# Kernel optimization log

Measured on AMD Instinct MI355X. Metric: run time of the kernel, lower is better.

## Reference

```python
import jax, jax.numpy as jnp
import numpy as np

B, S, H, F, E = 2, 2048, 1024, 4096, 8  # batch, seq, hidden, ffn, num_experts


def setup_inputs() -> dict:
    key = jax.random.key(0)
    ks = jax.random.split(key, 4)
    x = jax.random.normal(ks[0], (B, S, H), dtype=jnp.float32)
    w_router = jax.random.normal(ks[1], (H, E), dtype=jnp.float32) * 0.02
    w1 = jax.random.normal(ks[2], (E, H, F), dtype=jnp.float32) * 0.02
    b1 = jnp.zeros((E, F), dtype=jnp.float32)
    w2 = jax.random.normal(ks[3], (E, F, H), dtype=jnp.float32) * 0.02
    b2 = jnp.zeros((E, H), dtype=jnp.float32)
    return {"x": x, "w_router": w_router, "w1": w1, "b1": b1, "w2": w2, "b2": b2}


def reference(x, w_router, w1, b1, w2, b2):
    """Top-1 MoE layer: route -> per-expert FFN -> weighted combine.

    Faithful to ExpertParallelWrapper._process_moe_layer on a single group:
    router picks one expert per token with a routing weight; tokens are
    dispatched to experts (here expressed as a static mask over the fixed
    expert set), processed by the expert FFN, and scatter-combined back
    weighted by the routing probability.
    """
    Bs, Ss, Hs = x.shape
    n_experts = w1.shape[0]
    # Router: per-token logits -> softmax -> top-1 expert + weight
    logits = jnp.einsum('bsh,he->bse', x, w_router)          # [B,S,E]
    probs = jax.nn.softmax(logits, axis=-1)
    sel = jnp.argmax(probs, axis=-1)                          # [B,S] selected expert
    wgt = jnp.take_along_axis(probs, sel[..., None], axis=-1)[..., 0]  # [B,S]

    xt = x.reshape(-1, Hs)        # [T,H] flat tokens
    sel_t = sel.reshape(-1)       # [T]
    wgt_t = wgt.reshape(-1)       # [T]

    out = jnp.zeros_like(xt)
    # Static loop over the small fixed expert set (dispatch/combine via mask).
    for e in range(n_experts):
        h = jax.nn.relu(xt @ w1[e] + b1[e])   # [T,F]
        y = h @ w2[e] + b2[e]                 # [T,H]
        m = (sel_t == e).astype(xt.dtype) * wgt_t
        out = out + m[:, None] * y
    return out.reshape(Bs, Ss, Hs)
```

## Files before the change

kernel.cpp:

```cpp
#include <hip/hip_runtime.h>
#include <math.h>

#define T_TOK 4096
#define H_DIM 1024
#define F_DIM 4096
#define E_NUM 8
#define BK 64
#define KSPLIT 4

typedef __attribute__((ext_vector_type(8))) short bhalf8_t;
typedef __attribute__((ext_vector_type(8))) unsigned short ushort8_t;
typedef __attribute__((ext_vector_type(4))) float f32x4_t;

__device__ __forceinline__ unsigned short f2bf(float f) {
  unsigned int u = __float_as_uint(f);
  return (unsigned short)((u + 0x7fffu + ((u >> 16) & 1u)) >> 16);
}

__device__ __forceinline__ void gload16(const void* g, void* l) {
  __builtin_amdgcn_global_load_lds(
      (const __attribute__((address_space(1))) unsigned int*)g,
      (__attribute__((address_space(3))) unsigned int*)l, 16, 0, 0);
}

__device__ __forceinline__ void transpose_dev(const float* __restrict__ src,
                                              unsigned short* __restrict__ dst,
                                              int K, int N, int bx, int by, void* sm_) {
  float(*tile)[65] = (float(*)[65])sm_;
  const int n0 = bx * 64;
  const int k0 = by * 64;
  const int l = threadIdx.x;
  const int lr = l >> 4;
  const int lc = (l & 15) * 4;
#pragma unroll
  for (int i = 0; i < 64; i += 16) {
    const float4 v = *reinterpret_cast<const float4*>(&src[(size_t)(k0 + lr + i) * N + n0 + lc]);
    tile[lr + i][lc] = v.x;
    tile[lr + i][lc + 1] = v.y;
    tile[lr + i][lc + 2] = v.z;
    tile[lr + i][lc + 3] = v.w;
  }
  __syncthreads();
  const int kk = (l & 7) * 8;
  const int nr = l >> 3;
#pragma unroll
  for (int i = 0; i < 64; i += 32) {
    const int n = nr + i;
    ushort8_t o;
#pragma unroll
    for (int j = 0; j < 8; ++j) o[j] = f2bf(tile[kk + j][n]);
    *reinterpret_cast<ushort8_t*>(&dst[(size_t)(n0 + n) * K + k0 + kk]) = o;
  }
}

__global__ __launch_bounds__(256) void k_pre(const float* __restrict__ x,
                                             const float* __restrict__ wr,
                                             const float* __restrict__ w1,
                                             unsigned short* __restrict__ WT1,
                                             int* __restrict__ sel, float* __restrict__ wgt) {
  __shared__ __align__(16) char sm[64 * 65 * 4];
  if (blockIdx.x < 64) {
    transpose_dev(w1 + (size_t)blockIdx.z * H_DIM * F_DIM,
                  WT1 + (size_t)blockIdx.z * F_DIM * H_DIM,
                  H_DIM, F_DIM, blockIdx.x, blockIdx.y, sm);
    return;
  }
  if (blockIdx.z != 0) return;
  const int bid = blockIdx.y * 64 + (blockIdx.x - 64);
  const int t = bid * 4 + (threadIdx.x >> 6);
  const int lane = threadIdx.x & 63;
  const float* xr = x + (size_t)t * H_DIM;
  double acc[E_NUM] = {0, 0, 0, 0, 0, 0, 0, 0};
  for (int h = lane; h < H_DIM; h += 64) {
    const double xv = (double)xr[h];
    const float* w = wr + (size_t)h * E_NUM;
#pragma unroll
    for (int e = 0; e < E_NUM; ++e) acc[e] += xv * (double)w[e];
  }
#pragma unroll
  for (int e = 0; e < E_NUM; ++e) {
#pragma unroll
    for (int off = 32; off > 0; off >>= 1) acc[e] += __shfl_down(acc[e], off, 64);
  }
  if (lane == 0) {
    double m = acc[0];
    int a = 0;
#pragma unroll
    for (int e = 1; e < E_NUM; ++e)
      if (acc[e] > m) { m = acc[e]; a = e; }
    double s = 0.0;
#pragma unroll
    for (int e = 0; e < E_NUM; ++e) s += exp(acc[e] - m);
    sel[t] = a;
    wgt[t] = (float)(1.0 / s);
  }
}

__global__ void k_prefix(const int* __restrict__ sel, int* __restrict__ offs,
                         int* __restrict__ cursors) {
  __shared__ int h[E_NUM];
  if (threadIdx.x < E_NUM) h[threadIdx.x] = 0;
  __syncthreads();
  for (int i = threadIdx.x; i < T_TOK; i += 256) atomicAdd(&h[sel[i]], 1);
  __syncthreads();
  if (threadIdx.x == 0) {
    int s = 0;
    for (int e = 0; e < E_NUM; ++e) {
      offs[e] = s;
      cursors[e] = s;
      s += h[e];
    }
    offs[E_NUM] = s;
  }
}

__global__ void k_scatter(const float* __restrict__ x, const int* __restrict__ sel,
                          const float* __restrict__ wgt, int* __restrict__ cursors,
                          int* __restrict__ s2t, float* __restrict__ wgtS,
                          int* __restrict__ eS, unsigned short* __restrict__ Xs) {
  const int t = blockIdx.x;
  __shared__ int sslot;
  if (threadIdx.x == 0) {
    const int e = sel[t];
    const int slot = atomicAdd(&cursors[e], 1);
    sslot = slot;
    s2t[slot] = t;
    wgtS[slot] = wgt[t];
    eS[slot] = e;
  }
  __syncthreads();
  const int slot = sslot;
  const float4 v = reinterpret_cast<const float4*>(x + (size_t)t * H_DIM)[threadIdx.x];
  ushort4 o;
  o.x = f2bf(v.x); o.y = f2bf(v.y); o.z = f2bf(v.z); o.w = f2bf(v.w);
  reinterpret_cast<ushort4*>(Xs + (size_t)slot * H_DIM)[threadIdx.x] = o;
}

__global__ __launch_bounds__(256, 4) void k_mid(const unsigned short* __restrict__ Xs,
                                                const unsigned short* __restrict__ Wt,
                                                const float* __restrict__ b1,
                                                unsigned short* __restrict__ Hws,
                                                const int* __restrict__ offs,
                                                const float* __restrict__ w2,
                                                unsigned short* __restrict__ WT2) {
  __shared__ __align__(16) char sm[32768];
  if (blockIdx.x >= 32) {
    const int id = blockIdx.y * 32 + (blockIdx.x - 32);
    transpose_dev(w2 + (size_t)blockIdx.z * F_DIM * H_DIM,
                  WT2 + (size_t)blockIdx.z * H_DIM * F_DIM,
                  F_DIM, H_DIM, id & 15, id >> 4, sm);
    return;
  }
  const int e = blockIdx.z;
  const int off = offs[e];
  const int cnt = offs[e + 1] - off;
  const int m0 = blockIdx.y * 128;
  if (m0 >= cnt) return;
  const int n0 = blockIdx.x * 128;
  const int msize = cnt - m0;

  short* lA = (short*)sm;
  short* lB = (short*)(sm + 16384);

  const int tid = threadIdx.x;
  const int lane = tid & 63;
  const int wv = tid >> 6;
  const int wm = (wv >> 1) * 64;
  const int wn = (wv & 1) * 64;

  const int sRow = lane >> 3;
  const int cc = lane & 7;
  const int gch = cc ^ sRow;

  const unsigned short* Abase = Xs + (size_t)off * H_DIM;
  const unsigned short* Bbase = Wt + (size_t)e * F_DIM * H_DIM + (size_t)n0 * H_DIM;

  f32x4_t acc[4][4];
#pragma unroll
  for (int i = 0; i < 4; ++i)
#pragma unroll
    for (int j = 0; j < 4; ++j) acc[i][j] = (f32x4_t){0.f, 0.f, 0.f, 0.f};

  const int q = lane >> 4;
  const int r16 = lane & 15;
  const int sw = r16 & 7;

  for (int k0 = 0; k0 < H_DIM; k0 += BK) {
    __syncthreads();
#pragma unroll
    for (int i = 0; i < 4; ++i) {
      const int g = wv * 4 + i;
      const int row = g * 8 + sRow;
      const int ar = (row < msize) ? row : 0;
      gload16(Abase + (size_t)(m0 + ar) * H_DIM + k0 + gch * 8, &lA[g * 8 * BK]);
      gload16(Bbase + (size_t)row * H_DIM + k0 + gch * 8, &lB[g * 8 * BK]);
    }
    __syncthreads();

#pragma unroll
    for (int step = 0; step < 2; ++step) {
      const int slot = (step * 4 + q) ^ sw;
      bhalf8_t af[4], bf[4];
#pragma unroll
      for (int mi = 0; mi < 4; ++mi)
        af[mi] = *reinterpret_cast<const bhalf8_t*>(&lA[(wm + mi * 16 + r16) * BK + slot * 8]);
#pragma unroll
      for (int ni = 0; ni < 4; ++ni)
        bf[ni] = *reinterpret_cast<const bhalf8_t*>(&lB[(wn + ni * 16 + r16) * BK + slot * 8]);
#pragma unroll
      for (int mi = 0; mi < 4; ++mi)
#pragma unroll
        for (int ni = 0; ni < 4; ++ni)
          acc[mi][ni] = __builtin_amdgcn_mfma_f32_16x16x32_bf16(af[mi], bf[ni], acc[mi][ni], 0, 0, 0);
    }
  }

  const int c = lane & 15;
#pragma unroll
  for (int ni = 0; ni < 4; ++ni) {
    const int col = n0 + wn + ni * 16 + c;
    const float bias = b1[e * F_DIM + col];
#pragma unroll
    for (int mi = 0; mi < 4; ++mi) {
      const int rbase = wm + mi * 16 + q * 4;
#pragma unroll
      for (int r = 0; r < 4; ++r) {
        const int row = rbase + r;
        if (row < msize) {
          float v = acc[mi][ni][r] + bias;
          v = fmaxf(v, 0.0f);
          Hws[(size_t)(off + m0 + row) * F_DIM + col] = f2bf(v);
        }
      }
    }
  }
}

__global__ __launch_bounds__(256, 4) void k_ffn2_sk(const unsigned short* __restrict__ Hws,
                                                    const unsigned short* __restrict__ Wt,
                                                    const int* __restrict__ offs,
                                                    float* __restrict__ P) {
  const int e = blockIdx.z >> 2;
  const int ks = blockIdx.z & 3;
  const int off = offs[e];
  const int cnt = offs[e + 1] - off;
  const int m0 = blockIdx.y * 128;
  if (m0 >= cnt) return;
  const int n0 = blockIdx.x * 128;
  const int msize = cnt - m0;
  const int kbeg = ks * (F_DIM / KSPLIT);
  const int kend = kbeg + (F_DIM / KSPLIT);

  __shared__ short lA[128 * BK];
  __shared__ short lB[128 * BK];

  const int tid = threadIdx.x;
  const int lane = tid & 63;
  const int wv = tid >> 6;
  const int wm = (wv >> 1) * 64;
  const int wn = (wv & 1) * 64;

  const int sRow = lane >> 3;
  const int cc = lane & 7;
  const int gch = cc ^ sRow;

  const unsigned short* Abase = Hws + (size_t)off * F_DIM;
  const unsigned short* Bbase = Wt + (size_t)e * H_DIM * F_DIM + (size_t)n0 * F_DIM;

  f32x4_t acc[4][4];
#pragma unroll
  for (int i = 0; i < 4; ++i)
#pragma unroll
    for (int j = 0; j < 4; ++j) acc[i][j] = (f32x4_t){0.f, 0.f, 0.f, 0.f};

  const int q = lane >> 4;
  const int r16 = lane & 15;
  const int sw = r16 & 7;

  for (int k0 = kbeg; k0 < kend; k0 += BK) {
    __syncthreads();
#pragma unroll
    for (int i = 0; i < 4; ++i) {
      const int g = wv * 4 + i;
      const int row = g * 8 + sRow;
      const int ar = (row < msize) ? row : 0;
      gload16(Abase + (size_t)(m0 + ar) * F_DIM + k0 + gch * 8, &lA[g * 8 * BK]);
      gload16(Bbase + (size_t)row * F_DIM + k0 + gch * 8, &lB[g * 8 * BK]);
    }
    __syncthreads();

#pragma unroll
    for (int step = 0; step < 2; ++step) {
      const int slot = (step * 4 + q) ^ sw;
      bhalf8_t af[4], bf[4];
#pragma unroll
      for (int mi = 0; mi < 4; ++mi)
        af[mi] = *reinterpret_cast<const bhalf8_t*>(&lA[(wm + mi * 16 + r16) * BK + slot * 8]);
#pragma unroll
      for (int ni = 0; ni < 4; ++ni)
        bf[ni] = *reinterpret_cast<const bhalf8_t*>(&lB[(wn + ni * 16 + r16) * BK + slot * 8]);
#pragma unroll
      for (int mi = 0; mi < 4; ++mi)
#pragma unroll
        for (int ni = 0; ni < 4; ++ni)
          acc[mi][ni] = __builtin_amdgcn_mfma_f32_16x16x32_bf16(af[mi], bf[ni], acc[mi][ni], 0, 0, 0);
    }
  }

  const int c = lane & 15;
  float* Pb = P + (size_t)ks * T_TOK * H_DIM;
#pragma unroll
  for (int mi = 0; mi < 4; ++mi) {
    const int rbase = wm + mi * 16 + q * 4;
#pragma unroll
    for (int r = 0; r < 4; ++r) {
      const int row = rbase + r;
      if (row >= msize) continue;
      float* prow = Pb + (size_t)(off + m0 + row) * H_DIM;
#pragma unroll
      for (int ni = 0; ni < 4; ++ni) prow[n0 + wn + ni * 16 + c] = acc[mi][ni][r];
    }
  }
}

__global__ __launch_bounds__(256) void k_reduce(const float* __restrict__ P,
                                                const float* __restrict__ b2,
                                                const int* __restrict__ s2t,
                                                const int* __restrict__ eS,
                                                const float* __restrict__ wgtS,
                                                float* __restrict__ out) {
  const int srow = blockIdx.x;
  const int tok = s2t[srow];
  const int e = eS[srow];
  const float w = wgtS[srow];
  const int i = threadIdx.x;
  const size_t rowoff = (size_t)srow * H_DIM / 4 + i;
  const float4 p0 = reinterpret_cast<const float4*>(P)[rowoff];
  const float4 p1 = reinterpret_cast<const float4*>(P + (size_t)T_TOK * H_DIM)[rowoff];
  const float4 p2 = reinterpret_cast<const float4*>(P + (size_t)2 * T_TOK * H_DIM)[rowoff];
  const float4 p3 = reinterpret_cast<const float4*>(P + (size_t)3 * T_TOK * H_DIM)[rowoff];
  const float4 b = reinterpret_cast<const float4*>(b2 + (size_t)e * H_DIM)[i];
  float4 o;
  o.x = w * (p0.x + p1.x + p2.x + p3.x + b.x);
  o.y = w * (p0.y + p1.y + p2.y + p3.y + b.y);
  o.z = w * (p0.z + p1.z + p2.z + p3.z + b.z);
  o.w = w * (p0.w + p1.w + p2.w + p3.w + b.w);
  reinterpret_cast<float4*>(out + (size_t)tok * H_DIM)[i] = o;
}

__global__ __launch_bounds__(256) void k_transpose(const float* __restrict__ in,
                                                   unsigned short* __restrict__ out,
                                                   int K, int N) {
  __shared__ __align__(16) char sm[64 * 65 * 4];
  transpose_dev(in + (size_t)blockIdx.z * K * N, out + (size_t)blockIdx.z * N * K,
                K, N, blockIdx.x, blockIdx.y, sm);
}

__global__ __launch_bounds__(256, 4) void k_ffn2_direct(const unsigned short* __restrict__ Hws,
                                                        const unsigned short* __restrict__ Wt,
                                                        const float* __restrict__ b2,
                                                        const int* __restrict__ offs,
                                                        const int* __restrict__ s2t,
                                                        const float* __restrict__ wgtS,
                                                        float* __restrict__ out) {
  const int e = blockIdx.z;
  const int off = offs[e];
  const int cnt = offs[e + 1] - off;
  const int m0 = blockIdx.y * 128;
  if (m0 >= cnt) return;
  const int n0 = blockIdx.x * 128;
  const int msize = cnt - m0;

  __shared__ short lA[128 * BK];
  __shared__ short lB[128 * BK];

  const int tid = threadIdx.x;
  const int lane = tid & 63;
  const int wv = tid >> 6;
  const int wm = (wv >> 1) * 64;
  const int wn = (wv & 1) * 64;

  const int sRow = lane >> 3;
  const int cc = lane & 7;
  const int gch = cc ^ sRow;

  const unsigned short* Abase = Hws + (size_t)off * F_DIM;
  const unsigned short* Bbase = Wt + (size_t)e * H_DIM * F_DIM + (size_t)n0 * F_DIM;

  f32x4_t acc[4][4];
#pragma unroll
  for (int i = 0; i < 4; ++i)
#pragma unroll
    for (int j = 0; j < 4; ++j) acc[i][j] = (f32x4_t){0.f, 0.f, 0.f, 0.f};

  const int q = lane >> 4;
  const int r16 = lane & 15;
  const int sw = r16 & 7;

  for (int k0 = 0; k0 < F_DIM; k0 += BK) {
    __syncthreads();
#pragma unroll
    for (int i = 0; i < 4; ++i) {
      const int g = wv * 4 + i;
      const int row = g * 8 + sRow;
      const int ar = (row < msize) ? row : 0;
      gload16(Abase + (size_t)(m0 + ar) * F_DIM + k0 + gch * 8, &lA[g * 8 * BK]);
      gload16(Bbase + (size_t)row * F_DIM + k0 + gch * 8, &lB[g * 8 * BK]);
    }
    __syncthreads();

#pragma unroll
    for (int step = 0; step < 2; ++step) {
      const int slot = (step * 4 + q) ^ sw;
      bhalf8_t af[4], bf[4];
#pragma unroll
      for (int mi = 0; mi < 4; ++mi)
        af[mi] = *reinterpret_cast<const bhalf8_t*>(&lA[(wm + mi * 16 + r16) * BK + slot * 8]);
#pragma unroll
      for (int ni = 0; ni < 4; ++ni)
        bf[ni] = *reinterpret_cast<const bhalf8_t*>(&lB[(wn + ni * 16 + r16) * BK + slot * 8]);
#pragma unroll
      for (int mi = 0; mi < 4; ++mi)
#pragma unroll
        for (int ni = 0; ni < 4; ++ni)
          acc[mi][ni] = __builtin_amdgcn_mfma_f32_16x16x32_bf16(af[mi], bf[ni], acc[mi][ni], 0, 0, 0);
    }
  }

  const int c = lane & 15;
#pragma unroll
  for (int mi = 0; mi < 4; ++mi) {
    const int rbase = wm + mi * 16 + q * 4;
#pragma unroll
    for (int r = 0; r < 4; ++r) {
      const int row = rbase + r;
      if (row >= msize) continue;
      const int srow = off + m0 + row;
      const int tok = s2t[srow];
      const float w = wgtS[srow];
      float* orow = out + (size_t)tok * H_DIM;
#pragma unroll
      for (int ni = 0; ni < 4; ++ni) {
        const int col = n0 + wn + ni * 16 + c;
        orow[col] = w * (acc[mi][ni][r] + b2[e * H_DIM + col]);
      }
    }
  }
}

extern "C" void kernel_launch(void* const* d_in, const int* in_sizes, int n_in,
                              void* d_out, int out_size, void* d_ws, size_t ws_size,
                              hipStream_t stream) {
  const float* x  = (const float*)d_in[0];
  const float* wr = (const float*)d_in[1];
  const float* w1 = (const float*)d_in[2];
  const float* b1 = (const float*)d_in[3];
  const float* w2 = (const float*)d_in[4];
  const float* b2 = (const float*)d_in[5];
  float* out = (float*)d_out;

  char* ws = (char*)d_ws;
  const size_t NEED_FAST = 67108864ull * 2 + 8388608 + 33554432 + 98304;
  if (ws_size >= NEED_FAST) {
    unsigned short* WT1 = (unsigned short*)(ws);
    unsigned short* WT2 = (unsigned short*)(ws + 67108864);
    unsigned short* XS  = (unsigned short*)(ws + 134217728);
    unsigned short* HWS = (unsigned short*)(ws + 142606336);
    char* ctrl = ws + 176160768;
    int*   sel     = (int*)(ctrl);
    int*   s2t     = (int*)(ctrl + 16384);
    float* wgt     = (float*)(ctrl + 32768);
    float* wgtS    = (float*)(ctrl + 49152);
    int*   eS      = (int*)(ctrl + 65536);
    int*   offs    = (int*)(ctrl + 81920);
    int*   cursors = (int*)(ctrl + 81984);
    float* P = (float*)ws;

    k_pre<<<dim3(128, 16, 8), 256, 0, stream>>>(x, wr, w1, WT1, sel, wgt);
    k_prefix<<<1, 256, 0, stream>>>(sel, offs, cursors);
    k_scatter<<<T_TOK, 256, 0, stream>>>(x, sel, wgt, cursors, s2t, wgtS, eS, XS);
    k_mid<<<dim3(64, 32, 8), 256, 0, stream>>>(XS, WT1, b1, HWS, offs, w2, WT2);
    k_ffn2_sk<<<dim3(H_DIM / 128, T_TOK / 128, E_NUM * KSPLIT), 256, 0, stream>>>(HWS, WT2, offs, P);
    k_reduce<<<T_TOK, 256, 0, stream>>>(P, b2, s2t, eS, wgtS, out);
  } else {
    unsigned short* WT  = (unsigned short*)(ws);
    unsigned short* XS  = (unsigned short*)(ws + 67108864);
    unsigned short* HWS = (unsigned short*)(ws + 75497472);
    char* ctrl = ws + 109051904;
    int*   sel     = (int*)(ctrl);
    int*   s2t     = (int*)(ctrl + 16384);
    float* wgt     = (float*)(ctrl + 32768);
    float* wgtS    = (float*)(ctrl + 49152);
    int*   eS      = (int*)(ctrl + 65536);
    int*   offs    = (int*)(ctrl + 81920);
    int*   cursors = (int*)(ctrl + 81984);

    k_pre<<<dim3(128, 16, 8), 256, 0, stream>>>(x, wr, w1, WT, sel, wgt);
    k_prefix<<<1, 256, 0, stream>>>(sel, offs, cursors);
    k_scatter<<<T_TOK, 256, 0, stream>>>(x, sel, wgt, cursors, s2t, wgtS, eS, XS);
    k_mid<<<dim3(32, 32, 8), 256, 0, stream>>>(XS, WT, b1, HWS, offs, w2, (unsigned short*)0);
    k_transpose<<<dim3(H_DIM / 64, F_DIM / 64, E_NUM), 256, 0, stream>>>(w2, WT, F_DIM, H_DIM);
    k_ffn2_direct<<<dim3(H_DIM / 128, T_TOK / 128, E_NUM), 256, 0, stream>>>(HWS, WT, b2, offs, s2t, wgtS, out);
  }
}
```

Measured before the change: 500.7 us.

## Double-buffer LDS in FFN GEMMs, move w2 transpose into pre kernel, halve split-K

Both expert GEMM kernels now use two LDS buffers, so the next K tile is loaded while MFMAs run on the current one. They also raise wave priority during the MFMA section. The w2 transpose moves from the FFN1 kernel into the prologue kernel, alongside the w1 transpose and routing, so FFN1 becomes a pure GEMM. Split-K for FFN2 drops from 4 to 2, which halves the partial-sum traffic and the reduce work but gives fewer blocks. The doubled LDS lowers occupancy to 2 blocks per CU.

```diff
diff --git a/kernel.cpp b/kernel.cpp
--- a/kernel.cpp
+++ b/kernel.cpp
@@ -6,7 +6,7 @@
 #define F_DIM 4096
 #define E_NUM 8
 #define BK 64
-#define KSPLIT 4
+#define KSPLIT 2
 
 typedef __attribute__((ext_vector_type(8))) short bhalf8_t;
 typedef __attribute__((ext_vector_type(8))) unsigned short ushort8_t;
@@ -57,6 +57,8 @@
                                              const float* __restrict__ wr,
                                              const float* __restrict__ w1,
                                              unsigned short* __restrict__ WT1,
+                                             const float* __restrict__ w2,
+                                             unsigned short* __restrict__ WT2,
                                              int* __restrict__ sel, float* __restrict__ wgt) {
   __shared__ __align__(16) char sm[64 * 65 * 4];
   if (blockIdx.x < 64) {
@@ -65,8 +67,16 @@
                   H_DIM, F_DIM, blockIdx.x, blockIdx.y, sm);
     return;
   }
+  if (blockIdx.x < 128) {
+    if (WT2 == nullptr) return;
+    const int id = blockIdx.y * 64 + (blockIdx.x - 64);
+    transpose_dev(w2 + (size_t)blockIdx.z * F_DIM * H_DIM,
+                  WT2 + (size_t)blockIdx.z * H_DIM * F_DIM,
+                  F_DIM, H_DIM, id & 15, id >> 4, sm);
+    return;
+  }
   if (blockIdx.z != 0) return;
-  const int bid = blockIdx.y * 64 + (blockIdx.x - 64);
+  const int bid = blockIdx.y * 64 + (blockIdx.x - 128);
   const int t = bid * 4 + (threadIdx.x >> 6);
   const int lane = threadIdx.x & 63;
   const float* xr = x + (size_t)t * H_DIM;
@@ -136,21 +146,11 @@
   reinterpret_cast<ushort4*>(Xs + (size_t)slot * H_DIM)[threadIdx.x] = o;
 }
 
-__global__ __launch_bounds__(256, 4) void k_mid(const unsigned short* __restrict__ Xs,
-                                                const unsigned short* __restrict__ Wt,
-                                                const float* __restrict__ b1,
-                                                unsigned short* __restrict__ Hws,
-                                                const int* __restrict__ offs,
-                                                const float* __restrict__ w2,
-                                                unsigned short* __restrict__ WT2) {
-  __shared__ __align__(16) char sm[32768];
-  if (blockIdx.x >= 32) {
-    const int id = blockIdx.y * 32 + (blockIdx.x - 32);
-    transpose_dev(w2 + (size_t)blockIdx.z * F_DIM * H_DIM,
-                  WT2 + (size_t)blockIdx.z * H_DIM * F_DIM,
-                  F_DIM, H_DIM, id & 15, id >> 4, sm);
-    return;
-  }
+__global__ __launch_bounds__(256, 2) void k_ffn1(const unsigned short* __restrict__ Xs,
+                                                 const unsigned short* __restrict__ Wt,
+                                                 const float* __restrict__ b1,
+                                                 unsigned short* __restrict__ Hws,
+                                                 const int* __restrict__ offs) {
   const int e = blockIdx.z;
   const int off = offs[e];
   const int cnt = offs[e + 1] - off;
@@ -159,8 +159,8 @@
   const int n0 = blockIdx.x * 128;
   const int msize = cnt - m0;
 
-  short* lA = (short*)sm;
-  short* lB = (short*)(sm + 16384);
+  __shared__ short lA[2][128 * BK];
+  __shared__ short lB[2][128 * BK];
 
   const int tid = threadIdx.x;
   const int lane = tid & 63;
@@ -185,34 +185,44 @@
   const int r16 = lane & 15;
   const int sw = r16 & 7;
 
-  for (int k0 = 0; k0 < H_DIM; k0 += BK) {
-    __syncthreads();
+  auto stage = [&](int buf, int k0) {
 #pragma unroll
     for (int i = 0; i < 4; ++i) {
       const int g = wv * 4 + i;
       const int row = g * 8 + sRow;
       const int ar = (row < msize) ? row : 0;
-      gload16(Abase + (size_t)(m0 + ar) * H_DIM + k0 + gch * 8, &lA[g * 8 * BK]);
-      gload16(Bbase + (size_t)row * H_DIM + k0 + gch * 8, &lB[g * 8 * BK]);
-    }
-    __syncthreads();
-
+      gload16(Abase + (size_t)(m0 + ar) * H_DIM + k0 + gch * 8, &lA[buf][g * 8 * BK]);
+      gload16(Bbase + (size_t)row * H_DIM + k0 + gch * 8, &lB[buf][g * 8 * BK]);
+    }
+  };
+
+  stage(0, 0);
+  __syncthreads();
+  int cur = 0;
+  const int NT = H_DIM / BK;
+  for (int t = 0; t < NT; ++t) {
+    if (t + 1 < NT) stage(cur ^ 1, (t + 1) * BK);
+    __builtin_amdgcn_sched_barrier(0);
+    __builtin_amdgcn_s_setprio(1);
 #pragma unroll
     for (int step = 0; step < 2; ++step) {
       const int slot = (step * 4 + q) ^ sw;
       bhalf8_t af[4], bf[4];
 #pragma unroll
       for (int mi = 0; mi < 4; ++mi)
-        af[mi] = *reinterpret_cast<const bhalf8_t*>(&lA[(wm + mi * 16 + r16) * BK + slot * 8]);
+        af[mi] = *reinterpret_cast<const bhalf8_t*>(&lA[cur][(wm + mi * 16 + r16) * BK + slot * 8]);
 #pragma unroll
       for (int ni = 0; ni < 4; ++ni)
-        bf[ni] = *reinterpret_cast<const bhalf8_t*>(&lB[(wn + ni * 16 + r16) * BK + slot * 8]);
+        bf[ni] = *reinterpret_cast<const bhalf8_t*>(&lB[cur][(wn + ni * 16 + r16) * BK + slot * 8]);
 #pragma unroll
       for (int mi = 0; mi < 4; ++mi)
 #pragma unroll
         for (int ni = 0; ni < 4; ++ni)
           acc[mi][ni] = __builtin_amdgcn_mfma_f32_16x16x32_bf16(af[mi], bf[ni], acc[mi][ni], 0, 0, 0);
     }
+    __builtin_amdgcn_s_setprio(0);
+    __syncthreads();
+    cur ^= 1;
   }
 
   const int c = lane & 15;
@@ -236,12 +246,12 @@
   }
 }
 
-__global__ __launch_bounds__(256, 4) void k_ffn2_sk(const unsigned short* __restrict__ Hws,
+__global__ __launch_bounds__(256, 2) void k_ffn2_sk(const unsigned short* __restrict__ Hws,
                                                     const unsigned short* __restrict__ Wt,
                                                     const int* __restrict__ offs,
                                                     float* __restrict__ P) {
-  const int e = blockIdx.z >> 2;
-  const int ks = blockIdx.z & 3;
+  const int e = blockIdx.z >> 1;
+  const int ks = blockIdx.z & 1;
   const int off = offs[e];
   const int cnt = offs[e + 1] - off;
   const int m0 = blockIdx.y * 128;
@@ -249,10 +259,9 @@
   const int n0 = blockIdx.x * 128;
   const int msize = cnt - m0;
   const int kbeg = ks * (F_DIM / KSPLIT);
-  const int kend = kbeg + (F_DIM / KSPLIT);
-
-  __shared__ short lA[128 * BK];
-  __shared__ short lB[128 * BK];
+
+  __shared__ short lA[2][128 * BK];
+  __shared__ short lB[2][128 * BK];
 
   const int tid = threadIdx.x;
   const int lane = tid & 63;
@@ -277,34 +286,44 @@
   const int r16 = lane & 15;
   const int sw = r16 & 7;
 
-  for (int k0 = kbeg; k0 < kend; k0 += BK) {
-    __syncthreads();
+  auto stage = [&](int buf, int k0) {
 #pragma unroll
     for (int i = 0; i < 4; ++i) {
       const int g = wv * 4 + i;
       const int row = g * 8 + sRow;
       const int ar = (row < msize) ? row : 0;
-      gload16(Abase + (size_t)(m0 + ar) * F_DIM + k0 + gch * 8, &lA[g * 8 * BK]);
-      gload16(Bbase + (size_t)row * F_DIM + k0 + gch * 8, &lB[g * 8 * BK]);
-    }
-    __syncthreads();
-
+      gload16(Abase + (size_t)(m0 + ar) * F_DIM + k0 + gch * 8, &lA[buf][g * 8 * BK]);
+      gload16(Bbase + (size_t)row * F_DIM + k0 + gch * 8, &lB[buf][g * 8 * BK]);
+    }
+  };
+
+  stage(0, kbeg);
+  __syncthreads();
+  int cur = 0;
+  const int NT = (F_DIM / KSPLIT) / BK;
+  for (int t = 0; t < NT; ++t) {
+    if (t + 1 < NT) stage(cur ^ 1, kbeg + (t + 1) * BK);
+    __builtin_amdgcn_sched_barrier(0);
+    __builtin_amdgcn_s_setprio(1);
 #pragma unroll
     for (int step = 0; step < 2; ++step) {
       const int slot = (step * 4 + q) ^ sw;
       bhalf8_t af[4], bf[4];
 #pragma unroll
       for (int mi = 0; mi < 4; ++mi)
-        af[mi] = *reinterpret_cast<const bhalf8_t*>(&lA[(wm + mi * 16 + r16) * BK + slot * 8]);
+        af[mi] = *reinterpret_cast<const bhalf8_t*>(&lA[cur][(wm + mi * 16 + r16) * BK + slot * 8]);
 #pragma unroll
       for (int ni = 0; ni < 4; ++ni)
-        bf[ni] = *reinterpret_cast<const bhalf8_t*>(&lB[(wn + ni * 16 + r16) * BK + slot * 8]);
+        bf[ni] = *reinterpret_cast<const bhalf8_t*>(&lB[cur][(wn + ni * 16 + r16) * BK + slot * 8]);
 #pragma unroll
       for (int mi = 0; mi < 4; ++mi)
 #pragma unroll
         for (int ni = 0; ni < 4; ++ni)
           acc[mi][ni] = __builtin_amdgcn_mfma_f32_16x16x32_bf16(af[mi], bf[ni], acc[mi][ni], 0, 0, 0);
     }
+    __builtin_amdgcn_s_setprio(0);
+    __syncthreads();
+    cur ^= 1;
   }
 
   const int c = lane & 15;
@@ -337,14 +356,12 @@
   const size_t rowoff = (size_t)srow * H_DIM / 4 + i;
   const float4 p0 = reinterpret_cast<const float4*>(P)[rowoff];
   const float4 p1 = reinterpret_cast<const float4*>(P + (size_t)T_TOK * H_DIM)[rowoff];
-  const float4 p2 = reinterpret_cast<const float4*>(P + (size_t)2 * T_TOK * H_DIM)[rowoff];
-  const float4 p3 = reinterpret_cast<const float4*>(P + (size_t)3 * T_TOK * H_DIM)[rowoff];
   const float4 b = reinterpret_cast<const float4*>(b2 + (size_t)e * H_DIM)[i];
   float4 o;
-  o.x = w * (p0.x + p1.x + p2.x + p3.x + b.x);
-  o.y = w * (p0.y + p1.y + p2.y + p3.y + b.y);
-  o.z = w * (p0.z + p1.z + p2.z + p3.z + b.z);
-  o.w = w * (p0.w + p1.w + p2.w + p3.w + b.w);
+  o.x = w * (p0.x + p1.x + b.x);
+  o.y = w * (p0.y + p1.y + b.y);
+  o.z = w * (p0.z + p1.z + b.z);
+  o.w = w * (p0.w + p1.w + b.w);
   reinterpret_cast<float4*>(out + (size_t)tok * H_DIM)[i] = o;
 }
 
@@ -476,10 +493,10 @@
     int*   cursors = (int*)(ctrl + 81984);
     float* P = (float*)ws;
 
-    k_pre<<<dim3(128, 16, 8), 256, 0, stream>>>(x, wr, w1, WT1, sel, wgt);
+    k_pre<<<dim3(192, 16, 8), 256, 0, stream>>>(x, wr, w1, WT1, w2, WT2, sel, wgt);
     k_prefix<<<1, 256, 0, stream>>>(sel, offs, cursors);
     k_scatter<<<T_TOK, 256, 0, stream>>>(x, sel, wgt, cursors, s2t, wgtS, eS, XS);
-    k_mid<<<dim3(64, 32, 8), 256, 0, stream>>>(XS, WT1, b1, HWS, offs, w2, WT2);
+    k_ffn1<<<dim3(F_DIM / 128, T_TOK / 128, E_NUM), 256, 0, stream>>>(XS, WT1, b1, HWS, offs);
     k_ffn2_sk<<<dim3(H_DIM / 128, T_TOK / 128, E_NUM * KSPLIT), 256, 0, stream>>>(HWS, WT2, offs, P);
     k_reduce<<<T_TOK, 256, 0, stream>>>(P, b2, s2t, eS, wgtS, out);
   } else {
@@ -495,10 +512,10 @@
     int*   offs    = (int*)(ctrl + 81920);
     int*   cursors = (int*)(ctrl + 81984);
 
-    k_pre<<<dim3(128, 16, 8), 256, 0, stream>>>(x, wr, w1, WT, sel, wgt);
+    k_pre<<<dim3(192, 16, 8), 256, 0, stream>>>(x, wr, w1, WT, w2, (unsigned short*)0, sel, wgt);
     k_prefix<<<1, 256, 0, stream>>>(sel, offs, cursors);
     k_scatter<<<T_TOK, 256, 0, stream>>>(x, sel, wgt, cursors, s2t, wgtS, eS, XS);
-    k_mid<<<dim3(32, 32, 8), 256, 0, stream>>>(XS, WT, b1, HWS, offs, w2, (unsigned short*)0);
+    k_ffn1<<<dim3(F_DIM / 128, T_TOK / 128, E_NUM), 256, 0, stream>>>(XS, WT, b1, HWS, offs);
     k_transpose<<<dim3(H_DIM / 64, F_DIM / 64, E_NUM), 256, 0, stream>>>(w2, WT, F_DIM, H_DIM);
     k_ffn2_direct<<<dim3(H_DIM / 128, T_TOK / 128, E_NUM), 256, 0, stream>>>(HWS, WT, b2, offs, s2t, wgtS, out);
   }
```

New measurement: 536.6 us. +7.2%, slower.

## Move W2 transpose into pre-kernel and widen transpose tiles to 64x256

Applied to the files above, without the earlier changes.

Both weight transposes (W1 and W2) now run in the first kernel, interleaved with the router blocks through a flat 1D grid. The FFN1 GEMM kernel becomes a pure GEMM without transpose side-work. The transpose now handles 64x256 tiles, converts to bf16 before staging in LDS, and keeps 16 float4 loads in flight per thread, which cuts LDS traffic and raises memory-level parallelism. The risks are that the pre-kernel becomes heavier and no longer overlaps the W2 transpose with FFN1 compute, and that register pressure rises in the transpose.

```diff
diff --git a/kernel.cpp b/kernel.cpp
--- a/kernel.cpp
+++ b/kernel.cpp
@@ -23,33 +23,39 @@
       (__attribute__((address_space(3))) unsigned int*)l, 16, 0, 0);
 }
 
-__device__ __forceinline__ void transpose_dev(const float* __restrict__ src,
-                                              unsigned short* __restrict__ dst,
-                                              int K, int N, int bx, int by, void* sm_) {
-  float(*tile)[65] = (float(*)[65])sm_;
-  const int n0 = bx * 64;
-  const int k0 = by * 64;
-  const int l = threadIdx.x;
-  const int lr = l >> 4;
-  const int lc = (l & 15) * 4;
-#pragma unroll
-  for (int i = 0; i < 64; i += 16) {
-    const float4 v = *reinterpret_cast<const float4*>(&src[(size_t)(k0 + lr + i) * N + n0 + lc]);
-    tile[lr + i][lc] = v.x;
-    tile[lr + i][lc + 1] = v.y;
-    tile[lr + i][lc + 2] = v.z;
-    tile[lr + i][lc + 3] = v.w;
+#define TP_LDSTRIDE 260
+__device__ __forceinline__ void transpose_wide(const float* __restrict__ src,
+                                               unsigned short* __restrict__ dst,
+                                               int K, int N, int k0, int n0,
+                                               unsigned short* lds) {
+  const int t = threadIdx.x;
+  float4 v[16];
+#pragma unroll
+  for (int i = 0; i < 16; ++i) {
+    const int c = i * 256 + t;
+    const int row = c >> 6;
+    const int col = (c & 63) * 4;
+    v[i] = *reinterpret_cast<const float4*>(&src[(size_t)(k0 + row) * N + n0 + col]);
+  }
+#pragma unroll
+  for (int i = 0; i < 16; ++i) {
+    const int c = i * 256 + t;
+    const int row = c >> 6;
+    const int col = (c & 63) * 4;
+    ushort4 o;
+    o.x = f2bf(v[i].x); o.y = f2bf(v[i].y); o.z = f2bf(v[i].z); o.w = f2bf(v[i].w);
+    *reinterpret_cast<ushort4*>(&lds[row * TP_LDSTRIDE + col]) = o;
   }
   __syncthreads();
-  const int kk = (l & 7) * 8;
-  const int nr = l >> 3;
-#pragma unroll
-  for (int i = 0; i < 64; i += 32) {
-    const int n = nr + i;
+#pragma unroll
+  for (int i = 0; i < 8; ++i) {
+    const int oc = i * 256 + t;
+    const int n = oc >> 3;
+    const int c = oc & 7;
     ushort8_t o;
 #pragma unroll
-    for (int j = 0; j < 8; ++j) o[j] = f2bf(tile[kk + j][n]);
-    *reinterpret_cast<ushort8_t*>(&dst[(size_t)(n0 + n) * K + k0 + kk]) = o;
+    for (int j = 0; j < 8; ++j) o[j] = lds[(c * 8 + j) * TP_LDSTRIDE + n];
+    *reinterpret_cast<ushort8_t*>(&dst[(size_t)(n0 + n) * K + k0 + c * 8]) = o;
   }
 }
 
@@ -57,17 +63,31 @@
                                              const float* __restrict__ wr,
                                              const float* __restrict__ w1,
                                              unsigned short* __restrict__ WT1,
+                                             const float* __restrict__ w2,
+                                             unsigned short* __restrict__ WT2,
                                              int* __restrict__ sel, float* __restrict__ wgt) {
-  __shared__ __align__(16) char sm[64 * 65 * 4];
-  if (blockIdx.x < 64) {
-    transpose_dev(w1 + (size_t)blockIdx.z * H_DIM * F_DIM,
-                  WT1 + (size_t)blockIdx.z * F_DIM * H_DIM,
-                  H_DIM, F_DIM, blockIdx.x, blockIdx.y, sm);
+  __shared__ __align__(16) unsigned short lds[64 * TP_LDSTRIDE];
+  const unsigned int id = blockIdx.x;
+  const unsigned int r = id % 5u;
+  const unsigned int q = id / 5u;
+  if (r < 4u) {
+    const int tid4 = (int)(q * 4u + r);
+    if (tid4 < 2048) {
+      const int e = tid4 >> 8;
+      const int tt = tid4 & 255;
+      transpose_wide(w1 + (size_t)e * H_DIM * F_DIM, WT1 + (size_t)e * F_DIM * H_DIM,
+                     H_DIM, F_DIM, (tt >> 4) * 64, (tt & 15) * 256, lds);
+    } else {
+      if (WT2 == nullptr) return;
+      const int t2 = tid4 - 2048;
+      const int e = t2 >> 8;
+      const int tt = t2 & 255;
+      transpose_wide(w2 + (size_t)e * F_DIM * H_DIM, WT2 + (size_t)e * H_DIM * F_DIM,
+                     F_DIM, H_DIM, (tt >> 2) * 64, (tt & 3) * 256, lds);
+    }
     return;
   }
-  if (blockIdx.z != 0) return;
-  const int bid = blockIdx.y * 64 + (blockIdx.x - 64);
-  const int t = bid * 4 + (threadIdx.x >> 6);
+  const int t = (int)q * 4 + (threadIdx.x >> 6);
   const int lane = threadIdx.x & 63;
   const float* xr = x + (size_t)t * H_DIM;
   double acc[E_NUM] = {0, 0, 0, 0, 0, 0, 0, 0};
@@ -136,21 +156,11 @@
   reinterpret_cast<ushort4*>(Xs + (size_t)slot * H_DIM)[threadIdx.x] = o;
 }
 
-__global__ __launch_bounds__(256, 4) void k_mid(const unsigned short* __restrict__ Xs,
-                                                const unsigned short* __restrict__ Wt,
-                                                const float* __restrict__ b1,
-                                                unsigned short* __restrict__ Hws,
-                                                const int* __restrict__ offs,
-                                                const float* __restrict__ w2,
-                                                unsigned short* __restrict__ WT2) {
-  __shared__ __align__(16) char sm[32768];
-  if (blockIdx.x >= 32) {
-    const int id = blockIdx.y * 32 + (blockIdx.x - 32);
-    transpose_dev(w2 + (size_t)blockIdx.z * F_DIM * H_DIM,
-                  WT2 + (size_t)blockIdx.z * H_DIM * F_DIM,
-                  F_DIM, H_DIM, id & 15, id >> 4, sm);
-    return;
-  }
+__global__ __launch_bounds__(256, 4) void k_ffn1(const unsigned short* __restrict__ Xs,
+                                                 const unsigned short* __restrict__ Wt,
+                                                 const float* __restrict__ b1,
+                                                 unsigned short* __restrict__ Hws,
+                                                 const int* __restrict__ offs) {
   const int e = blockIdx.z;
   const int off = offs[e];
   const int cnt = offs[e + 1] - off;
@@ -159,8 +169,8 @@
   const int n0 = blockIdx.x * 128;
   const int msize = cnt - m0;
 
-  short* lA = (short*)sm;
-  short* lB = (short*)(sm + 16384);
+  __shared__ short lA[128 * BK];
+  __shared__ short lB[128 * BK];
 
   const int tid = threadIdx.x;
   const int lane = tid & 63;
@@ -348,6 +358,36 @@
   reinterpret_cast<float4*>(out + (size_t)tok * H_DIM)[i] = o;
 }
 
+__device__ __forceinline__ void transpose_dev(const float* __restrict__ src,
+                                              unsigned short* __restrict__ dst,
+                                              int K, int N, int bx, int by, void* sm_) {
+  float(*tile)[65] = (float(*)[65])sm_;
+  const int n0 = bx * 64;
+  const int k0 = by * 64;
+  const int l = threadIdx.x;
+  const int lr = l >> 4;
+  const int lc = (l & 15) * 4;
+#pragma unroll
+  for (int i = 0; i < 64; i += 16) {
+    const float4 v = *reinterpret_cast<const float4*>(&src[(size_t)(k0 + lr + i) * N + n0 + lc]);
+    tile[lr + i][lc] = v.x;
+    tile[lr + i][lc + 1] = v.y;
+    tile[lr + i][lc + 2] = v.z;
+    tile[lr + i][lc + 3] = v.w;
+  }
+  __syncthreads();
+  const int kk = (l & 7) * 8;
+  const int nr = l >> 3;
+#pragma unroll
+  for (int i = 0; i < 64; i += 32) {
+    const int n = nr + i;
+    ushort8_t o;
+#pragma unroll
+    for (int j = 0; j < 8; ++j) o[j] = f2bf(tile[kk + j][n]);
+    *reinterpret_cast<ushort8_t*>(&dst[(size_t)(n0 + n) * K + k0 + kk]) = o;
+  }
+}
+
 __global__ __launch_bounds__(256) void k_transpose(const float* __restrict__ in,
                                                    unsigned short* __restrict__ out,
                                                    int K, int N) {
@@ -476,10 +516,10 @@
     int*   cursors = (int*)(ctrl + 81984);
     float* P = (float*)ws;
 
-    k_pre<<<dim3(128, 16, 8), 256, 0, stream>>>(x, wr, w1, WT1, sel, wgt);
+    k_pre<<<5120, 256, 0, stream>>>(x, wr, w1, WT1, w2, WT2, sel, wgt);
     k_prefix<<<1, 256, 0, stream>>>(sel, offs, cursors);
     k_scatter<<<T_TOK, 256, 0, stream>>>(x, sel, wgt, cursors, s2t, wgtS, eS, XS);
-    k_mid<<<dim3(64, 32, 8), 256, 0, stream>>>(XS, WT1, b1, HWS, offs, w2, WT2);
+    k_ffn1<<<dim3(F_DIM / 128, T_TOK / 128, E_NUM), 256, 0, stream>>>(XS, WT1, b1, HWS, offs);
     k_ffn2_sk<<<dim3(H_DIM / 128, T_TOK / 128, E_NUM * KSPLIT), 256, 0, stream>>>(HWS, WT2, offs, P);
     k_reduce<<<T_TOK, 256, 0, stream>>>(P, b2, s2t, eS, wgtS, out);
   } else {
@@ -495,10 +535,10 @@
     int*   offs    = (int*)(ctrl + 81920);
     int*   cursors = (int*)(ctrl + 81984);
 
-    k_pre<<<dim3(128, 16, 8), 256, 0, stream>>>(x, wr, w1, WT, sel, wgt);
+    k_pre<<<5120, 256, 0, stream>>>(x, wr, w1, WT, w2, (unsigned short*)0, sel, wgt);
     k_prefix<<<1, 256, 0, stream>>>(sel, offs, cursors);
     k_scatter<<<T_TOK, 256, 0, stream>>>(x, sel, wgt, cursors, s2t, wgtS, eS, XS);
-    k_mid<<<dim3(32, 32, 8), 256, 0, stream>>>(XS, WT, b1, HWS, offs, w2, (unsigned short*)0);
+    k_ffn1<<<dim3(F_DIM / 128, T_TOK / 128, E_NUM), 256, 0, stream>>>(XS, WT, b1, HWS, offs);
     k_transpose<<<dim3(H_DIM / 64, F_DIM / 64, E_NUM), 256, 0, stream>>>(w2, WT, F_DIM, H_DIM);
     k_ffn2_direct<<<dim3(H_DIM / 128, T_TOK / 128, E_NUM), 256, 0, stream>>>(HWS, WT, b2, offs, s2t, wgtS, out);
   }
```

Result: slower. 513.0 us (+2.4%).

## Compact MoE launch grids with a tile list and fold slot assignment into prefix

Applied to the files above, without the earlier changes.

The prefix kernel now assigns sorted slots to tokens itself and builds a list of occupied (expert, m-tile) pairs. The FFN2 split-K kernel launches over that compact list instead of a full expert-by-m-tile grid that mostly exits early. k_pre interleaves router blocks among transpose blocks in a flat 1D grid, and the scatter and reduce kernels each handle four rows per block. The goal is to cut empty block launches and per-token block overhead, at the cost of a serial slot-assignment pass inside a single block.

```diff
diff --git a/kernel.cpp b/kernel.cpp
--- a/kernel.cpp
+++ b/kernel.cpp
@@ -7,6 +7,7 @@
 #define E_NUM 8
 #define BK 64
 #define KSPLIT 4
+#define MT_MAX 40
 
 typedef __attribute__((ext_vector_type(8))) short bhalf8_t;
 typedef __attribute__((ext_vector_type(8))) unsigned short ushort8_t;
@@ -53,87 +54,111 @@
   }
 }
 
+__device__ __forceinline__ void router_body(const float* __restrict__ x,
+                                            const float* __restrict__ wr,
+                                            int t, int* __restrict__ sel,
+                                            float* __restrict__ wgt) {
+  const int lane = threadIdx.x & 63;
+  const float* xr = x + (size_t)t * H_DIM;
+  double acc[E_NUM] = {0, 0, 0, 0, 0, 0, 0, 0};
+  for (int h = lane; h < H_DIM; h += 64) {
+    const double xv = (double)xr[h];
+    const float* w = wr + (size_t)h * E_NUM;
+#pragma unroll
+    for (int e = 0; e < E_NUM; ++e) acc[e] += xv * (double)w[e];
+  }
+#pragma unroll
+  for (int e = 0; e < E_NUM; ++e) {
+#pragma unroll
+    for (int off = 32; off > 0; off >>= 1) acc[e] += __shfl_down(acc[e], off, 64);
+  }
+  if (lane == 0) {
+    double m = acc[0];
+    int a = 0;
+#pragma unroll
+    for (int e = 1; e < E_NUM; ++e)
+      if (acc[e] > m) { m = acc[e]; a = e; }
+    double s = 0.0;
+#pragma unroll
+    for (int e = 0; e < E_NUM; ++e) s += exp(acc[e] - m);
+    sel[t] = a;
+    wgt[t] = (float)(1.0 / s);
+  }
+}
+
 __global__ __launch_bounds__(256) void k_pre(const float* __restrict__ x,
                                              const float* __restrict__ wr,
                                              const float* __restrict__ w1,
                                              unsigned short* __restrict__ WT1,
                                              int* __restrict__ sel, float* __restrict__ wgt) {
   __shared__ __align__(16) char sm[64 * 65 * 4];
-  if (blockIdx.x < 64) {
-    transpose_dev(w1 + (size_t)blockIdx.z * H_DIM * F_DIM,
-                  WT1 + (size_t)blockIdx.z * F_DIM * H_DIM,
-                  H_DIM, F_DIM, blockIdx.x, blockIdx.y, sm);
+  const unsigned int id = blockIdx.x;
+  const unsigned int r = id % 9u;
+  const unsigned int q = id / 9u;
+  if (r < 8u) {
+    const int tile = (int)(q * 8u + r);
+    const int e = tile >> 10;
+    const int tt = tile & 1023;
+    transpose_dev(w1 + (size_t)e * H_DIM * F_DIM, WT1 + (size_t)e * F_DIM * H_DIM,
+                  H_DIM, F_DIM, tt & 63, tt >> 6, sm);
     return;
   }
-  if (blockIdx.z != 0) return;
-  const int bid = blockIdx.y * 64 + (blockIdx.x - 64);
-  const int t = bid * 4 + (threadIdx.x >> 6);
-  const int lane = threadIdx.x & 63;
-  const float* xr = x + (size_t)t * H_DIM;
-  double acc[E_NUM] = {0, 0, 0, 0, 0, 0, 0, 0};
-  for (int h = lane; h < H_DIM; h += 64) {
-    const double xv = (double)xr[h];
-    const float* w = wr + (size_t)h * E_NUM;
-#pragma unroll
-    for (int e = 0; e < E_NUM; ++e) acc[e] += xv * (double)w[e];
-  }
-#pragma unroll
-  for (int e = 0; e < E_NUM; ++e) {
-#pragma unroll
-    for (int off = 32; off > 0; off >>= 1) acc[e] += __shfl_down(acc[e], off, 64);
-  }
-  if (lane == 0) {
-    double m = acc[0];
-    int a = 0;
-#pragma unroll
-    for (int e = 1; e < E_NUM; ++e)
-      if (acc[e] > m) { m = acc[e]; a = e; }
-    double s = 0.0;
-#pragma unroll
-    for (int e = 0; e < E_NUM; ++e) s += exp(acc[e] - m);
-    sel[t] = a;
-    wgt[t] = (float)(1.0 / s);
-  }
-}
-
-__global__ void k_prefix(const int* __restrict__ sel, int* __restrict__ offs,
-                         int* __restrict__ cursors) {
+  router_body(x, wr, (int)q * 4 + (threadIdx.x >> 6), sel, wgt);
+}
+
+__global__ __launch_bounds__(256) void k_prefix(const int* __restrict__ sel,
+                                                const float* __restrict__ wgt,
+                                                int* __restrict__ offs,
+                                                int* __restrict__ s2t,
+                                                float* __restrict__ wgtS,
+                                                int* __restrict__ eS,
+                                                int* __restrict__ mtE,
+                                                int* __restrict__ mtM,
+                                                int* __restrict__ nmt) {
   __shared__ int h[E_NUM];
-  if (threadIdx.x < E_NUM) h[threadIdx.x] = 0;
+  __shared__ int cur[E_NUM];
+  const int tid = threadIdx.x;
+  if (tid < E_NUM) h[tid] = 0;
   __syncthreads();
-  for (int i = threadIdx.x; i < T_TOK; i += 256) atomicAdd(&h[sel[i]], 1);
+  for (int i = tid; i < T_TOK; i += 256) atomicAdd(&h[sel[i]], 1);
   __syncthreads();
-  if (threadIdx.x == 0) {
-    int s = 0;
+  if (tid == 0) {
+    int s = 0, m = 0;
     for (int e = 0; e < E_NUM; ++e) {
       offs[e] = s;
-      cursors[e] = s;
+      cur[e] = s;
+      for (int m0 = 0; m0 < h[e]; m0 += 128) { mtE[m] = e; mtM[m] = m0; ++m; }
       s += h[e];
     }
     offs[E_NUM] = s;
-  }
-}
-
-__global__ void k_scatter(const float* __restrict__ x, const int* __restrict__ sel,
-                          const float* __restrict__ wgt, int* __restrict__ cursors,
-                          int* __restrict__ s2t, float* __restrict__ wgtS,
-                          int* __restrict__ eS, unsigned short* __restrict__ Xs) {
-  const int t = blockIdx.x;
-  __shared__ int sslot;
-  if (threadIdx.x == 0) {
+    *nmt = m;
+  }
+  __syncthreads();
+  for (int t = tid; t < T_TOK; t += 256) {
     const int e = sel[t];
-    const int slot = atomicAdd(&cursors[e], 1);
-    sslot = slot;
+    const int slot = atomicAdd(&cur[e], 1);
     s2t[slot] = t;
     wgtS[slot] = wgt[t];
     eS[slot] = e;
   }
-  __syncthreads();
-  const int slot = sslot;
-  const float4 v = reinterpret_cast<const float4*>(x + (size_t)t * H_DIM)[threadIdx.x];
-  ushort4 o;
-  o.x = f2bf(v.x); o.y = f2bf(v.y); o.z = f2bf(v.z); o.w = f2bf(v.w);
-  reinterpret_cast<ushort4*>(Xs + (size_t)slot * H_DIM)[threadIdx.x] = o;
+}
+
+__global__ __launch_bounds__(256) void k_scatter(const float* __restrict__ x,
+                                                 const int* __restrict__ s2t,
+                                                 unsigned short* __restrict__ Xs) {
+  const int wv = threadIdx.x >> 6;
+  const int lane = threadIdx.x & 63;
+  const int slot = blockIdx.x * 4 + wv;
+  const int t = s2t[slot];
+  const float4* xr = reinterpret_cast<const float4*>(x + (size_t)t * H_DIM);
+  ushort4* xo = reinterpret_cast<ushort4*>(Xs + (size_t)slot * H_DIM);
+#pragma unroll
+  for (int kx = 0; kx < 4; ++kx) {
+    const float4 v = xr[lane + kx * 64];
+    ushort4 o;
+    o.x = f2bf(v.x); o.y = f2bf(v.y); o.z = f2bf(v.z); o.w = f2bf(v.w);
+    xo[lane + kx * 64] = o;
+  }
 }
 
 __global__ __launch_bounds__(256, 4) void k_mid(const unsigned short* __restrict__ Xs,
@@ -236,23 +261,18 @@
   }
 }
 
-__global__ __launch_bounds__(256, 4) void k_ffn2_sk(const unsigned short* __restrict__ Hws,
-                                                    const unsigned short* __restrict__ Wt,
-                                                    const int* __restrict__ offs,
-                                                    float* __restrict__ P) {
-  const int e = blockIdx.z >> 2;
-  const int ks = blockIdx.z & 3;
+__device__ __forceinline__ void ffn2_item(const unsigned short* __restrict__ Hws,
+                                          const unsigned short* __restrict__ Wt,
+                                          const int* __restrict__ offs,
+                                          float* __restrict__ P,
+                                          int e, int m0, int n0, int ks) {
+  __shared__ short lA[128 * BK];
+  __shared__ short lB[128 * BK];
   const int off = offs[e];
   const int cnt = offs[e + 1] - off;
-  const int m0 = blockIdx.y * 128;
-  if (m0 >= cnt) return;
-  const int n0 = blockIdx.x * 128;
   const int msize = cnt - m0;
   const int kbeg = ks * (F_DIM / KSPLIT);
   const int kend = kbeg + (F_DIM / KSPLIT);
-
-  __shared__ short lA[128 * BK];
-  __shared__ short lB[128 * BK];
 
   const int tid = threadIdx.x;
   const int lane = tid & 63;
@@ -323,29 +343,44 @@
   }
 }
 
+__global__ __launch_bounds__(256, 4) void k_ffn2_sk(const unsigned short* __restrict__ Hws,
+                                                    const unsigned short* __restrict__ Wt,
+                                                    const int* __restrict__ offs,
+                                                    float* __restrict__ P,
+                                                    const int* __restrict__ mtE,
+                                                    const int* __restrict__ mtM,
+                                                    const int* __restrict__ nmt) {
+  const int mt = blockIdx.y;
+  if (mt >= *nmt) return;
+  ffn2_item(Hws, Wt, offs, P, mtE[mt], mtM[mt], blockIdx.x * 128, blockIdx.z);
+}
+
 __global__ __launch_bounds__(256) void k_reduce(const float* __restrict__ P,
                                                 const float* __restrict__ b2,
                                                 const int* __restrict__ s2t,
                                                 const int* __restrict__ eS,
                                                 const float* __restrict__ wgtS,
                                                 float* __restrict__ out) {
-  const int srow = blockIdx.x;
-  const int tok = s2t[srow];
-  const int e = eS[srow];
-  const float w = wgtS[srow];
   const int i = threadIdx.x;
-  const size_t rowoff = (size_t)srow * H_DIM / 4 + i;
-  const float4 p0 = reinterpret_cast<const float4*>(P)[rowoff];
-  const float4 p1 = reinterpret_cast<const float4*>(P + (size_t)T_TOK * H_DIM)[rowoff];
-  const float4 p2 = reinterpret_cast<const float4*>(P + (size_t)2 * T_TOK * H_DIM)[rowoff];
-  const float4 p3 = reinterpret_cast<const float4*>(P + (size_t)3 * T_TOK * H_DIM)[rowoff];
-  const float4 b = reinterpret_cast<const float4*>(b2 + (size_t)e * H_DIM)[i];
-  float4 o;
-  o.x = w * (p0.x + p1.x + p2.x + p3.x + b.x);
-  o.y = w * (p0.y + p1.y + p2.y + p3.y + b.y);
-  o.z = w * (p0.z + p1.z + p2.z + p3.z + b.z);
-  o.w = w * (p0.w + p1.w + p2.w + p3.w + b.w);
-  reinterpret_cast<float4*>(out + (size_t)tok * H_DIM)[i] = o;
+#pragma unroll 1
+  for (int j = 0; j < 4; ++j) {
+    const int srow = blockIdx.x * 4 + j;
+    const int tok = s2t[srow];
+    const int e = eS[srow];
+    const float w = wgtS[srow];
+    const size_t rowoff = (size_t)srow * H_DIM / 4 + i;
+    const float4 p0 = reinterpret_cast<const float4*>(P)[rowoff];
+    const float4 p1 = reinterpret_cast<const float4*>(P + (size_t)T_TOK * H_DIM)[rowoff];
+    const float4 p2 = reinterpret_cast<const float4*>(P + (size_t)2 * T_TOK * H_DIM)[rowoff];
+    const float4 p3 = reinterpret_cast<const float4*>(P + (size_t)3 * T_TOK * H_DIM)[rowoff];
+    const float4 b = reinterpret_cast<const float4*>(b2 + (size_t)e * H_DIM)[i];
+    float4 o;
+    o.x = w * (p0.x + p1.x + p2.x + p3.x + b.x);
+    o.y = w * (p0.y + p1.y + p2.y + p3.y + b.y);
+    o.z = w * (p0.z + p1.z + p2.z + p3.z + b.z);
+    o.w = w * (p0.w + p1.w + p2.w + p3.w + b.w);
+    reinterpret_cast<float4*>(out + (size_t)tok * H_DIM)[i] = o;
+  }
 }
 
 __global__ __launch_bounds__(256) void k_transpose(const float* __restrict__ in,
@@ -473,15 +508,17 @@
     float* wgtS    = (float*)(ctrl + 49152);
     int*   eS      = (int*)(ctrl + 65536);
     int*   offs    = (int*)(ctrl + 81920);
-    int*   cursors = (int*)(ctrl + 81984);
+    int*   mtE     = (int*)(ctrl + 82048);
+    int*   mtM     = (int*)(ctrl + 82304);
+    int*   nmt     = (int*)(ctrl + 82560);
     float* P = (float*)ws;
 
-    k_pre<<<dim3(128, 16, 8), 256, 0, stream>>>(x, wr, w1, WT1, sel, wgt);
-    k_prefix<<<1, 256, 0, stream>>>(sel, offs, cursors);
-    k_scatter<<<T_TOK, 256, 0, stream>>>(x, sel, wgt, cursors, s2t, wgtS, eS, XS);
+    k_pre<<<9216, 256, 0, stream>>>(x, wr, w1, WT1, sel, wgt);
+    k_prefix<<<1, 256, 0, stream>>>(sel, wgt, offs, s2t, wgtS, eS, mtE, mtM, nmt);
+    k_scatter<<<T_TOK / 4, 256, 0, stream>>>(x, s2t, XS);
     k_mid<<<dim3(64, 32, 8), 256, 0, stream>>>(XS, WT1, b1, HWS, offs, w2, WT2);
-    k_ffn2_sk<<<dim3(H_DIM / 128, T_TOK / 128, E_NUM * KSPLIT), 256, 0, stream>>>(HWS, WT2, offs, P);
-    k_reduce<<<T_TOK, 256, 0, stream>>>(P, b2, s2t, eS, wgtS, out);
+    k_ffn2_sk<<<dim3(H_DIM / 128, MT_MAX, KSPLIT), 256, 0, stream>>>(HWS, WT2, offs, P, mtE, mtM, nmt);
+    k_reduce<<<T_TOK / 4, 256, 0, stream>>>(P, b2, s2t, eS, wgtS, out);
   } else {
     unsigned short* WT  = (unsigned short*)(ws);
     unsigned short* XS  = (unsigned short*)(ws + 67108864);
@@ -493,11 +530,13 @@
     float* wgtS    = (float*)(ctrl + 49152);
     int*   eS      = (int*)(ctrl + 65536);
     int*   offs    = (int*)(ctrl + 81920);
-    int*   cursors = (int*)(ctrl + 81984);
-
-    k_pre<<<dim3(128, 16, 8), 256, 0, stream>>>(x, wr, w1, WT, sel, wgt);
-    k_prefix<<<1, 256, 0, stream>>>(sel, offs, cursors);
-    k_scatter<<<T_TOK, 256, 0, stream>>>(x, sel, wgt, cursors, s2t, wgtS, eS, XS);
+    int*   mtE     = (int*)(ctrl + 82048);
+    int*   mtM     = (int*)(ctrl + 82304);
+    int*   nmt     = (int*)(ctrl + 82560);
+
+    k_pre<<<9216, 256, 0, stream>>>(x, wr, w1, WT, sel, wgt);
+    k_prefix<<<1, 256, 0, stream>>>(sel, wgt, offs, s2t, wgtS, eS, mtE, mtM, nmt);
+    k_scatter<<<T_TOK / 4, 256, 0, stream>>>(x, s2t, XS);
     k_mid<<<dim3(32, 32, 8), 256, 0, stream>>>(XS, WT, b1, HWS, offs, w2, (unsigned short*)0);
     k_transpose<<<dim3(H_DIM / 64, F_DIM / 64, E_NUM), 256, 0, stream>>>(w2, WT, F_DIM, H_DIM);
     k_ffn2_direct<<<dim3(H_DIM / 128, T_TOK / 128, E_NUM), 256, 0, stream>>>(HWS, WT, b2, offs, s2t, wgtS, out);
```

After: 471.3 us. -5.9%, faster.
